# Kernel optimization log

Hardware: AMD Instinct MI355X
Metric: run time of the kernel (lower is better)

The kernel has to match this reference:

```python
import jax, jax.numpy as jnp
import numpy as np

B, E, LC, LE, D = 32, 8, 256, 512, 256   # batch, evi_num, claim_len, evidence_len, emb_dim
OUT, H = 128, 1                          # attention hidden dim, head_num
NEG = -1e18


def setup_inputs() -> dict:
    key = jax.random.key(0)
    ks = jax.random.split(key, 8)
    claim = jax.random.normal(ks[0], (B, E, LC, D), jnp.float32)
    evidence = jax.random.normal(ks[1], (B, E, LE, D), jnp.float32)
    claim_len_mask = jax.random.randint(ks[2], (B, E, 1, LC), 0, 2).astype(jnp.int32)
    evidence_len_mask = jax.random.randint(ks[3], (B, E, 1, LE), 0, 2).astype(jnp.int32)
    s2d = 1.0 / np.sqrt(2 * D)
    so = 1.0 / np.sqrt(OUT)
    W1 = jax.random.normal(ks[4], (2 * D, OUT), jnp.float32) * s2d  # torch W1.weight.T
    w2 = jax.random.normal(ks[5], (OUT, H), jnp.float32) * so
    W2 = jax.random.normal(ks[6], (2 * D, OUT), jnp.float32) * s2d
    w1 = jax.random.normal(ks[7], (OUT, H), jnp.float32) * so
    return {"claim": claim, "claim_len_mask": claim_len_mask,
            "evidence": evidence, "evidence_len_mask": evidence_len_mask,
            "W1": W1, "w2": w2, "W2": W2, "w1": w1}


def _pooled_attend(seq, seq_mask, pooled, W, w):
    # seq: (B,E,L,D), pooled: (B,E,1,D), W: (2D,OUT), w: (OUT,H)
    # cat([seq, pooled_expanded]) @ W  ==  seq @ W[:D] + pooled @ W[D:]  (broadcast)
    h = jnp.tanh(seq @ W[:D] + pooled @ W[D:])          # (B,E,L,OUT)
    att = h @ w                                          # (B,E,L,H)
    mask = jnp.swapaxes(seq_mask, -1, -2).astype(bool)   # (B,E,L,1), broadcast over H
    att = jnp.where(mask, att, NEG)
    scores = jax.nn.softmax(att, axis=-2)                # softmax over L
    out = jnp.einsum('belh,beld->behd', scores, seq)     # (B,E,H,D)
    return out.reshape(out.shape[0], out.shape[1], 1, -1)  # (B,E,1,H*D)


def reference(claim, claim_len_mask, evidence, evidence_len_mask, W1, w2, W2, w1):
    c_mean = jnp.mean(claim, axis=-2, keepdims=True)     # (B,E,1,D)
    e_hat = _pooled_attend(evidence, evidence_len_mask, c_mean, W1, w2)
    e_mean = jnp.mean(evidence, axis=-2, keepdims=True)  # (B,E,1,D)
    c_hat = _pooled_attend(claim, claim_len_mask, e_mean, W2, w1)
    return c_hat, e_hat
```

## Files before the change

### kernel.cpp

```cpp
#include <hip/hip_runtime.h>
#include <hip/hip_bf16.h>
#include <math.h>

#define BE   256
#define DIM  256
#define OUTD 128
#define LCL  256
#define LEV  512
#define NEGV -1e18f

typedef short  bf16x8  __attribute__((ext_vector_type(8)));
typedef float  floatx4 __attribute__((ext_vector_type(4)));

union BF1 { __hip_bfloat16 h; unsigned short u; };
union BF2 { __hip_bfloat162 h; unsigned int u; };

__device__ __forceinline__ float fast_tanh(float x) {
    float xc = fminf(fmaxf(x, -15.f), 15.f);
    float e = __expf(2.f * xc);
    return (e - 1.f) * __builtin_amdgcn_rcpf(e + 1.f);
}

__device__ __forceinline__ void gl_lds16(const float4* g, float4* l) {
    __builtin_amdgcn_global_load_lds(
        (const __attribute__((address_space(1))) unsigned int*)(const void*)g,
        (__attribute__((address_space(3))) unsigned int*)(void*)l,
        16, 0, 0);
}

__global__ __launch_bounds__(512) void k_meanbias(
    const float* __restrict__ claim, const float* __restrict__ evidence,
    const float* __restrict__ W1, const float* __restrict__ W2,
    float* __restrict__ bias_e, float* __restrict__ bias_c,
    unsigned short* __restrict__ WT1, unsigned short* __restrict__ WT2)
{
    const int bid = blockIdx.x;
    const int t = threadIdx.x;
    if (bid >= BE) {
        const int side = bid - BE;
        const float* W = side ? W2 : W1;
        unsigned short* WT = side ? WT2 : WT1;
        for (int i = t; i < OUTD * DIM; i += 512) {
            const int d = i & (DIM - 1);
            const int n = i >> 8;
            BF1 c; c.h = __float2bfloat16(W[(size_t)d * OUTD + n]);
            WT[n * DIM + d] = c.u;
        }
        return;
    }
    const int pair = bid;
    const int d4 = t & 63, rg = t >> 6;
    __shared__ float4 smc[8][64];
    __shared__ float4 sme[8][64];
    __shared__ float mc[DIM], me[DIM];
    __shared__ float sb[2][2][OUTD];

    const float4* c4 = (const float4*)(claim + (size_t)pair * LCL * DIM);
    const float4* e4 = (const float4*)(evidence + (size_t)pair * LEV * DIM);
    float4 ac = make_float4(0.f, 0.f, 0.f, 0.f);
    float4 ae = make_float4(0.f, 0.f, 0.f, 0.f);
#pragma unroll 8
    for (int r = rg; r < LCL; r += 8) {
        const float4 v = c4[r * 64 + d4];
        ac.x += v.x; ac.y += v.y; ac.z += v.z; ac.w += v.w;
    }
#pragma unroll 8
    for (int r = rg; r < LEV; r += 8) {
        const float4 v = e4[r * 64 + d4];
        ae.x += v.x; ae.y += v.y; ae.z += v.z; ae.w += v.w;
    }
    smc[rg][d4] = ac; sme[rg][d4] = ae;
    __syncthreads();
    if (t < 64) {
        float4 s = make_float4(0.f, 0.f, 0.f, 0.f);
#pragma unroll
        for (int j = 0; j < 8; ++j) {
            const float4 v = smc[j][t];
            s.x += v.x; s.y += v.y; s.z += v.z; s.w += v.w;
        }
        ((float4*)mc)[t] = make_float4(s.x * (1.f / LCL), s.y * (1.f / LCL),
                                       s.z * (1.f / LCL), s.w * (1.f / LCL));
    } else if (t < 128) {
        const int u = t - 64;
        float4 s = make_float4(0.f, 0.f, 0.f, 0.f);
#pragma unroll
        for (int j = 0; j < 8; ++j) {
            const float4 v = sme[j][u];
            s.x += v.x; s.y += v.y; s.z += v.z; s.w += v.w;
        }
        ((float4*)me)[u] = make_float4(s.x * (1.f / LEV), s.y * (1.f / LEV),
                                       s.z * (1.f / LEV), s.w * (1.f / LEV));
    }
    __syncthreads();
    const int side = t >> 8, o = t & 127, dh = (t >> 7) & 1;
    const float* W = side ? W2 : W1;
    const float* m = side ? me : mc;
    float s = 0.f;
#pragma unroll 8
    for (int i = 0; i < 128; ++i) {
        const int d = dh * 128 + i;
        s += m[d] * W[(size_t)(DIM + d) * OUTD + o];
    }
    sb[side][dh][o] = s;
    __syncthreads();
    if (t < 256) {
        const int sd = t >> 7, oo = t & 127;
        const float bv = sb[sd][0][oo] + sb[sd][1][oo];
        (sd ? bias_c : bias_e)[pair * OUTD + oo] = bv;
    }
}

__global__ __launch_bounds__(512) void k_fused(
    const float* __restrict__ claim, const float* __restrict__ evidence,
    const unsigned short* __restrict__ WT1, const unsigned short* __restrict__ WT2,
    const float* __restrict__ w2v, const float* __restrict__ w1v,
    const float* __restrict__ bias_e, const float* __restrict__ bias_c,
    const int* __restrict__ emask, const int* __restrict__ cmask,
    float* __restrict__ out)
{
    constexpr int SR4 = 65;
    __shared__ float4 sA4[2][64 * SR4];
    __shared__ float sred[64][2];
    __shared__ float patt[64];
    __shared__ float stats[2];

    const int bid = blockIdx.x;
    const bool is_ev = (bid & 1) == 0;
    const int pair = bid >> 1;
    const float* __restrict__ seq  = is_ev ? evidence : claim;
    const unsigned short* __restrict__ WT = is_ev ? WT1 : WT2;
    const float* __restrict__ wvec = is_ev ? w2v : w1v;
    const float* __restrict__ bias = is_ev ? bias_e : bias_c;
    const int*   __restrict__ mask = is_ev ? emask : cmask;
    float* __restrict__ outp       = is_ev ? out + (size_t)BE * DIM : out;
    const int L  = is_ev ? LEV : LCL;
    const int NT = L >> 6;

    const int t = threadIdx.x;
    const int lane = t & 63;
    const int wv = t >> 6;
    const int wrow = wv >> 1;
    const int wcolg = wv & 1;
    const int q = lane >> 4, c16 = lane & 15;
    const int d4 = t & 63, rg = t >> 6;

    float bc[4], wc[4];
#pragma unroll
    for (int ct = 0; ct < 4; ++ct) {
        const int col = wcolg * 64 + ct * 16 + c16;
        bc[ct] = bias[pair * OUTD + col];
        wc[ct] = wvec[col];
    }
    const unsigned short* wbase = WT + (size_t)(wcolg * 64 + c16) * DIM + q * 8;
    const float4* sp4 = (const float4*)(seq + (size_t)pair * L * DIM);

    auto stage = [&](int buf, int tile) {
        const float4* base = sp4 + (size_t)tile * 4096;
#pragma unroll
        for (int j = 0; j < 8; ++j) {
            const int row = wv * 8 + j;
            gl_lds16(base + row * 64 + lane, &sA4[buf][row * SR4]);
        }
    };

    stage(0, 0);
    int cur = 0;

    float4 Oac = make_float4(0.f, 0.f, 0.f, 0.f);
    float m_run = -INFINITY, l_run = 0.f;

    for (int tile = 0; tile < NT; ++tile) {
        __syncthreads();
        if (tile + 1 < NT) stage(cur ^ 1, tile + 1);

        floatx4 acc[4];
#pragma unroll
        for (int ct = 0; ct < 4; ++ct) acc[ct] = (floatx4){0.f, 0.f, 0.f, 0.f};
        const int arow = wrow * 16 + c16;
#pragma unroll
        for (int ks = 0; ks < 8; ++ks) {
            bf16x8 bfr[4];
#pragma unroll
            for (int ct = 0; ct < 4; ++ct)
                bfr[ct] = *(const bf16x8*)(wbase + (size_t)ct * 16 * DIM + ks * 32);
            const float4 lo = sA4[cur][arow * SR4 + ks * 8 + q * 2];
            const float4 hi = sA4[cur][arow * SR4 + ks * 8 + q * 2 + 1];
            union { bf16x8 v; BF2 p[4]; } ua;
            ua.p[0].h = __float22bfloat162_rn(make_float2(lo.x, lo.y));
            ua.p[1].h = __float22bfloat162_rn(make_float2(lo.z, lo.w));
            ua.p[2].h = __float22bfloat162_rn(make_float2(hi.x, hi.y));
            ua.p[3].h = __float22bfloat162_rn(make_float2(hi.z, hi.w));
#pragma unroll
            for (int ct = 0; ct < 4; ++ct)
                acc[ct] = __builtin_amdgcn_mfma_f32_16x16x32_bf16(ua.v, bfr[ct], acc[ct], 0, 0, 0);
        }

#pragma unroll
        for (int reg = 0; reg < 4; ++reg) {
            float s = 0.f;
#pragma unroll
            for (int ct = 0; ct < 4; ++ct)
                s += fast_tanh(acc[ct][reg] + bc[ct]) * wc[ct];
#pragma unroll
            for (int off = 1; off < 16; off <<= 1) s += __shfl_xor(s, off, 64);
            if (c16 == 0)
                sred[wrow * 16 + q * 4 + reg][wcolg] = s;
        }
        __syncthreads();

        if (t < 64) {
            float a = sred[t][0] + sred[t][1];
            a = mask[pair * L + tile * 64 + t] ? a : NEGV;
            float mx = a;
#pragma unroll
            for (int off = 1; off < 64; off <<= 1) mx = fmaxf(mx, __shfl_xor(mx, off, 64));
            const float newm = fmaxf(m_run, mx);
            const float e = expf(a - newm);
            patt[t] = e;
            float sm = e;
#pragma unroll
            for (int off = 1; off < 64; off <<= 1) sm += __shfl_xor(sm, off, 64);
            if (t == 0) { stats[0] = newm; stats[1] = sm; }
        }
        __syncthreads();
        const float newm = stats[0], tsum = stats[1];
        const float scale = expf(m_run - newm);
        l_run = l_run * scale + tsum;
        m_run = newm;
        Oac.x *= scale; Oac.y *= scale; Oac.z *= scale; Oac.w *= scale;

#pragma unroll
        for (int r = 0; r < 8; ++r) {
            const float pl = patt[rg * 8 + r];
            const float4 v = sA4[cur][(rg * 8 + r) * SR4 + d4];
            Oac.x += pl * v.x; Oac.y += pl * v.y; Oac.z += pl * v.z; Oac.w += pl * v.w;
        }
        cur ^= 1;
    }

    __syncthreads();
    ((float4*)sA4)[t] = Oac;
    __syncthreads();
    if (t < 64) {
        float4 s = make_float4(0.f, 0.f, 0.f, 0.f);
#pragma unroll
        for (int j = 0; j < 8; ++j) {
            const float4 v = ((float4*)sA4)[j * 64 + t];
            s.x += v.x; s.y += v.y; s.z += v.z; s.w += v.w;
        }
        const float inv = 1.f / l_run;
        ((float4*)(outp + (size_t)pair * DIM))[t] =
            make_float4(s.x * inv, s.y * inv, s.z * inv, s.w * inv);
    }
}

extern "C" void kernel_launch(void* const* d_in, const int* in_sizes, int n_in,
                              void* d_out, int out_size, void* d_ws, size_t ws_size,
                              hipStream_t stream) {
    const float* claim    = (const float*)d_in[0];
    const int*   cmask    = (const int*)  d_in[1];
    const float* evidence = (const float*)d_in[2];
    const int*   emask    = (const int*)  d_in[3];
    const float* W1       = (const float*)d_in[4];
    const float* w2       = (const float*)d_in[5];
    const float* W2       = (const float*)d_in[6];
    const float* w1       = (const float*)d_in[7];
    float* out = (float*)d_out;

    float* ws = (float*)d_ws;
    float* bias_e = ws;
    float* bias_c = bias_e + BE * OUTD;
    unsigned short* WT1 = (unsigned short*)(bias_c + BE * OUTD);
    unsigned short* WT2 = WT1 + OUTD * DIM;

    k_meanbias<<<BE + 2, 512, 0, stream>>>(claim, evidence, W1, W2,
                                           bias_e, bias_c, WT1, WT2);
    k_fused<<<2 * BE, 512, 0, stream>>>(claim, evidence, WT1, WT2, w2, w1,
                                        bias_e, bias_c, emask, cmask, out);
}
```

Before: 349.6 us.

## Halve tile rows, redistribute waves, replace softmax LDS stage with per-wave shuffles

Tiles shrink from 64 to 32 rows, so LDS per block halves and a launch bound of two blocks per CU becomes possible. Waves are regrouped into 2 row groups by 4 column groups. Every wave now computes the tile's online-softmax statistics redundantly with wave shuffles, which removes the patt/stats LDS arrays and one block barrier per tile. Raw s_barrier with explicit waitcnt replaces __syncthreads, and fast __expf replaces expf. The cost is twice as many tile iterations and barriers, plus redundant softmax work in every wave.

Result: slower. 399.9 us (+14.4%).

```diff
diff --git a/kernel.cpp b/kernel.cpp
--- a/kernel.cpp
+++ b/kernel.cpp
@@ -110,7 +110,7 @@
     }
 }
 
-__global__ __launch_bounds__(512) void k_fused(
+__global__ __launch_bounds__(512, 2) void k_fused(
     const float* __restrict__ claim, const float* __restrict__ evidence,
     const unsigned short* __restrict__ WT1, const unsigned short* __restrict__ WT2,
     const float* __restrict__ w2v, const float* __restrict__ w1v,
@@ -118,11 +118,10 @@
     const int* __restrict__ emask, const int* __restrict__ cmask,
     float* __restrict__ out)
 {
+    constexpr int TR  = 32;
     constexpr int SR4 = 65;
-    __shared__ float4 sA4[2][64 * SR4];
-    __shared__ float sred[64][2];
-    __shared__ float patt[64];
-    __shared__ float stats[2];
+    __shared__ float4 sA4[2][TR * SR4];
+    __shared__ float sred[TR][4];
 
     const int bid = blockIdx.x;
     const bool is_ev = (bid & 1) == 0;
@@ -134,31 +133,30 @@
     const int*   __restrict__ mask = is_ev ? emask : cmask;
     float* __restrict__ outp       = is_ev ? out + (size_t)BE * DIM : out;
     const int L  = is_ev ? LEV : LCL;
-    const int NT = L >> 6;
+    const int NT = L >> 5;
 
     const int t = threadIdx.x;
     const int lane = t & 63;
     const int wv = t >> 6;
-    const int wrow = wv >> 1;
-    const int wcolg = wv & 1;
+    const int wrowf = wv >> 2;
+    const int wcg = wv & 3;
     const int q = lane >> 4, c16 = lane & 15;
-    const int d4 = t & 63, rg = t >> 6;
-
-    float bc[4], wc[4];
-#pragma unroll
-    for (int ct = 0; ct < 4; ++ct) {
-        const int col = wcolg * 64 + ct * 16 + c16;
+
+    float bc[2], wc[2];
+#pragma unroll
+    for (int ct = 0; ct < 2; ++ct) {
+        const int col = wcg * 32 + ct * 16 + c16;
         bc[ct] = bias[pair * OUTD + col];
         wc[ct] = wvec[col];
     }
-    const unsigned short* wbase = WT + (size_t)(wcolg * 64 + c16) * DIM + q * 8;
+    const unsigned short* wbase = WT + (size_t)(wcg * 32 + c16) * DIM + q * 8;
     const float4* sp4 = (const float4*)(seq + (size_t)pair * L * DIM);
 
     auto stage = [&](int buf, int tile) {
-        const float4* base = sp4 + (size_t)tile * 4096;
-#pragma unroll
-        for (int j = 0; j < 8; ++j) {
-            const int row = wv * 8 + j;
+        const float4* base = sp4 + (size_t)tile * (TR * 64);
+#pragma unroll
+        for (int j = 0; j < 4; ++j) {
+            const int row = wv * 4 + j;
             gl_lds16(base + row * 64 + lane, &sA4[buf][row * SR4]);
         }
     };
@@ -170,18 +168,19 @@
     float m_run = -INFINITY, l_run = 0.f;
 
     for (int tile = 0; tile < NT; ++tile) {
-        __syncthreads();
+        asm volatile("s_waitcnt vmcnt(0) lgkmcnt(0)" ::: "memory");
+        __builtin_amdgcn_s_barrier();
         if (tile + 1 < NT) stage(cur ^ 1, tile + 1);
 
-        floatx4 acc[4];
-#pragma unroll
-        for (int ct = 0; ct < 4; ++ct) acc[ct] = (floatx4){0.f, 0.f, 0.f, 0.f};
-        const int arow = wrow * 16 + c16;
+        floatx4 acc[2];
+        acc[0] = (floatx4){0.f, 0.f, 0.f, 0.f};
+        acc[1] = (floatx4){0.f, 0.f, 0.f, 0.f};
+        const int arow = wrowf * 16 + c16;
 #pragma unroll
         for (int ks = 0; ks < 8; ++ks) {
-            bf16x8 bfr[4];
-#pragma unroll
-            for (int ct = 0; ct < 4; ++ct)
+            bf16x8 bfr[2];
+#pragma unroll
+            for (int ct = 0; ct < 2; ++ct)
                 bfr[ct] = *(const bf16x8*)(wbase + (size_t)ct * 16 * DIM + ks * 32);
             const float4 lo = sA4[cur][arow * SR4 + ks * 8 + q * 2];
             const float4 hi = sA4[cur][arow * SR4 + ks * 8 + q * 2 + 1];
@@ -191,7 +190,7 @@
             ua.p[2].h = __float22bfloat162_rn(make_float2(hi.x, hi.y));
             ua.p[3].h = __float22bfloat162_rn(make_float2(hi.z, hi.w));
 #pragma unroll
-            for (int ct = 0; ct < 4; ++ct)
+            for (int ct = 0; ct < 2; ++ct)
                 acc[ct] = __builtin_amdgcn_mfma_f32_16x16x32_bf16(ua.v, bfr[ct], acc[ct], 0, 0, 0);
         }
 
@@ -199,40 +198,37 @@
         for (int reg = 0; reg < 4; ++reg) {
             float s = 0.f;
 #pragma unroll
-            for (int ct = 0; ct < 4; ++ct)
+            for (int ct = 0; ct < 2; ++ct)
                 s += fast_tanh(acc[ct][reg] + bc[ct]) * wc[ct];
 #pragma unroll
             for (int off = 1; off < 16; off <<= 1) s += __shfl_xor(s, off, 64);
             if (c16 == 0)
-                sred[wrow * 16 + q * 4 + reg][wcolg] = s;
-        }
-        __syncthreads();
-
-        if (t < 64) {
-            float a = sred[t][0] + sred[t][1];
-            a = mask[pair * L + tile * 64 + t] ? a : NEGV;
-            float mx = a;
-#pragma unroll
-            for (int off = 1; off < 64; off <<= 1) mx = fmaxf(mx, __shfl_xor(mx, off, 64));
-            const float newm = fmaxf(m_run, mx);
-            const float e = expf(a - newm);
-            patt[t] = e;
-            float sm = e;
-#pragma unroll
-            for (int off = 1; off < 64; off <<= 1) sm += __shfl_xor(sm, off, 64);
-            if (t == 0) { stats[0] = newm; stats[1] = sm; }
-        }
-        __syncthreads();
-        const float newm = stats[0], tsum = stats[1];
-        const float scale = expf(m_run - newm);
-        l_run = l_run * scale + tsum;
+                sred[wrowf * 16 + q * 4 + reg][wcg] = s;
+        }
+        asm volatile("s_waitcnt lgkmcnt(0)" ::: "memory");
+        __builtin_amdgcn_s_barrier();
+
+        const int row = lane & 31;
+        float a = sred[row][0] + sred[row][1] + sred[row][2] + sred[row][3];
+        a = mask[pair * L + tile * TR + row] ? a : NEGV;
+        float mx = a;
+#pragma unroll
+        for (int off = 1; off < 64; off <<= 1) mx = fmaxf(mx, __shfl_xor(mx, off, 64));
+        const float newm = fmaxf(m_run, mx);
+        const float e = __expf(a - newm);
+        float sm = e;
+#pragma unroll
+        for (int off = 1; off < 64; off <<= 1) sm += __shfl_xor(sm, off, 64);
+        const float scale = __expf(m_run - newm);
+        l_run = l_run * scale + 0.5f * sm;
         m_run = newm;
         Oac.x *= scale; Oac.y *= scale; Oac.z *= scale; Oac.w *= scale;
 
 #pragma unroll
-        for (int r = 0; r < 8; ++r) {
-            const float pl = patt[rg * 8 + r];
-            const float4 v = sA4[cur][(rg * 8 + r) * SR4 + d4];
+        for (int r = 0; r < 4; ++r) {
+            const int rw = wv * 4 + r;
+            const float pl = __shfl(e, rw, 64);
+            const float4 v = sA4[cur][rw * SR4 + lane];
             Oac.x += pl * v.x; Oac.y += pl * v.y; Oac.z += pl * v.z; Oac.w += pl * v.w;
         }
         cur ^= 1;
```
